# Kernel optimization log

Measured on AMD Instinct MI355X. Metric: run time of the kernel, lower is better.

The kernel has to match this reference:

```python
import jax, jax.numpy as jnp
import numpy as np

P = 2            # config['p']
BLUR = 0.05      # config['blur']
SCALING = 0.5    # config['scaling']
N_STEPS = 20     # static upper bound on the eps-annealing schedule length

N_D, N_S, D_IN, D_OUT = 2048, 1024, 768, 64


def setup_inputs() -> dict:
    key = jax.random.key(0)
    k1, k2, k3 = jax.random.split(key, 3)
    d = jax.random.normal(k1, (N_D, D_IN), dtype=jnp.float32)
    s = jax.random.normal(k2, (N_S, D_IN), dtype=jnp.float32)
    # learned projection; small init so distances (and thus the loss) stay O(1-10)
    M = 0.02 * jax.random.normal(k3, (D_IN, D_OUT), dtype=jnp.float32)
    return {"d": d, "s": s, "M": M}


def _cost(x, y):
    # geomloss p=2 cost: C(x,y) = ||x - y||^2 / 2
    x2 = jnp.sum(x * x, axis=1)[:, None]
    y2 = jnp.sum(y * y, axis=1)[None, :]
    return 0.5 * (x2 + y2 - 2.0 * (x @ y.T))


def _softmin(eps, C, h):
    # h = eps*log_weights + dual potential, shape [M]; C shape [N, M]
    return -eps * jax.nn.logsumexp((h[None, :] - C) / eps, axis=1)


def _sinkhorn_divergence(x, y):
    Na, Nb = x.shape[0], y.shape[0]
    log_a = jnp.full((Na,), -jnp.log(float(Na)), dtype=x.dtype)  # uniform weights
    log_b = jnp.full((Nb,), -jnp.log(float(Nb)), dtype=x.dtype)

    C_xy = _cost(x, y)
    C_yx = C_xy.T
    C_xx = _cost(x, x)
    C_yy = _cost(y, y)

    # geomloss max_diameter: norm of per-dim range over the union of clouds
    mins = jnp.minimum(x.min(0), y.min(0))
    maxs = jnp.maximum(x.max(0), y.max(0))
    diameter = jnp.sqrt(jnp.sum((maxs - mins) ** 2))

    # eps-scaling schedule: diameter^p -> blur^p, geometric decay by scaling^p,
    # padded to static length N_STEPS (extra steps just refine at eps=blur^p)
    t = jnp.arange(N_STEPS, dtype=x.dtype)
    eps_list = jnp.maximum((diameter ** P) * (SCALING ** P) ** t, BLUR ** P)

    eps0 = eps_list[0]
    f_ab = _softmin(eps0, C_xy, eps0 * log_b)
    g_ab = _softmin(eps0, C_yx, eps0 * log_a)
    f_aa = _softmin(eps0, C_xx, eps0 * log_a)
    g_bb = _softmin(eps0, C_yy, eps0 * log_b)

    def step(carry, eps):
        f_ab, g_ab, f_aa, g_bb = carry
        ft = _softmin(eps, C_xy, eps * log_b + g_ab)
        gt = _softmin(eps, C_yx, eps * log_a + f_ab)
        f_aa = 0.5 * (f_aa + _softmin(eps, C_xx, eps * log_a + f_aa))
        g_bb = 0.5 * (g_bb + _softmin(eps, C_yy, eps * log_b + g_bb))
        return (0.5 * (f_ab + ft), 0.5 * (g_ab + gt), f_aa, g_bb), None

    (f_ab, g_ab, f_aa, g_bb), _ = jax.lax.scan(step, (f_ab, g_ab, f_aa, g_bb), eps_list)

    # final non-averaged extrapolation step at eps = blur^p
    eps = jnp.asarray(BLUR ** P, dtype=x.dtype)
    f_ab = _softmin(eps, C_xy, eps * log_b + g_ab)
    g_ab = _softmin(eps, C_yx, eps * log_a + f_ab)
    f_aa = _softmin(eps, C_xx, eps * log_a + f_aa)
    g_bb = _softmin(eps, C_yy, eps * log_b + g_bb)

    # debiased Sinkhorn divergence: <a, f_ab - f_aa> + <b, g_ab - g_bb>
    return jnp.mean(f_ab - f_aa) + jnp.mean(g_ab - g_bb)


def reference(d, s, M):
    x = d @ M  # [N_d, D_out]
    y = s @ M  # [N_s, D_out]
    loss = _sinkhorn_divergence(x, y)
    return jnp.exp(-loss)
```

## Files before the change

### kernel.cpp

```cpp
#include <hip/hip_runtime.h>
#include <hip/hip_fp16.h>
#include <math.h>

#define ND 2048
#define NS 1024
#define DIN 768
#define DOUT 64
#define NSTEPS 20
static constexpr float BLUR2 = 0.05f * 0.05f;

#define OFF_X     0u
#define OFF_MM    199680u
#define OFF_POTS  199808u
#define POT_STRIDE 6144u
#define OFF_BARRIER 341120u
#define H_DXY 694528u
#define H_DYX 2791680u
#define H_DXX 4888832u
#define H_DYY 9083136u

#define NBLK 1152

__device__ inline unsigned fkey(float f) {
  const unsigned b = __float_as_uint(f);
  return (b & 0x80000000u) ? ~b : (b | 0x80000000u);
}
__device__ inline float funkey(unsigned k) {
  const unsigned b = (k & 0x80000000u) ? (k & 0x7FFFFFFFu) : ~k;
  return __uint_as_float(b);
}

__global__ __launch_bounds__(256) void init_mm(float* __restrict__ ws) {
  const int t = threadIdx.x;
  unsigned* mm = reinterpret_cast<unsigned*>(ws + OFF_MM);
  if (t < 64)       mm[t] = 0xFFFFFFFFu;
  else if (t < 128) mm[t] = 0u;
  unsigned* bar = reinterpret_cast<unsigned*>(ws + OFF_BARRIER);
  for (int i = t; i < 6144; i += 256) bar[i] = 0u;
}

__global__ __launch_bounds__(256) void proj_kernel(const float* __restrict__ d,
                                                   const float* __restrict__ s,
                                                   const float* __restrict__ M,
                                                   float* __restrict__ ws) {
  const int w    = threadIdx.x >> 6;
  const int lane = threadIdx.x & 63;
  const int r0   = blockIdx.x * 4;

  const float* base;
  if (r0 < ND) base = d + (size_t)r0 * DIN;
  else         base = s + (size_t)(r0 - ND) * DIN;

  const float4* s0 = reinterpret_cast<const float4*>(base + 0 * DIN + w * 192);
  const float4* s1 = reinterpret_cast<const float4*>(base + 1 * DIN + w * 192);
  const float4* s2 = reinterpret_cast<const float4*>(base + 2 * DIN + w * 192);
  const float4* s3 = reinterpret_cast<const float4*>(base + 3 * DIN + w * 192);
  const float* Mw = M + (size_t)(w * 192) * DOUT + lane;

  float a0 = 0.f, a1 = 0.f, a2 = 0.f, a3 = 0.f;
#pragma unroll 4
  for (int kk = 0; kk < 48; ++kk) {
    const float4 r0v = s0[kk];
    const float4 r1v = s1[kk];
    const float4 r2v = s2[kk];
    const float4 r3v = s3[kk];
    const float m0 = Mw[(kk * 4 + 0) * DOUT];
    const float m1 = Mw[(kk * 4 + 1) * DOUT];
    const float m2 = Mw[(kk * 4 + 2) * DOUT];
    const float m3 = Mw[(kk * 4 + 3) * DOUT];
    a0 = fmaf(r0v.x, m0, a0); a0 = fmaf(r0v.y, m1, a0);
    a0 = fmaf(r0v.z, m2, a0); a0 = fmaf(r0v.w, m3, a0);
    a1 = fmaf(r1v.x, m0, a1); a1 = fmaf(r1v.y, m1, a1);
    a1 = fmaf(r1v.z, m2, a1); a1 = fmaf(r1v.w, m3, a1);
    a2 = fmaf(r2v.x, m0, a2); a2 = fmaf(r2v.y, m1, a2);
    a2 = fmaf(r2v.z, m2, a2); a2 = fmaf(r2v.w, m3, a2);
    a3 = fmaf(r3v.x, m0, a3); a3 = fmaf(r3v.y, m1, a3);
    a3 = fmaf(r3v.z, m2, a3); a3 = fmaf(r3v.w, m3, a3);
  }

  __shared__ float part[4][4][64];
  part[w][0][lane] = a0;
  part[w][1][lane] = a1;
  part[w][2][lane] = a2;
  part[w][3][lane] = a3;
  __syncthreads();

  if (w == 0) {
    const float f0 = part[0][0][lane] + part[1][0][lane] + part[2][0][lane] + part[3][0][lane];
    const float f1 = part[0][1][lane] + part[1][1][lane] + part[2][1][lane] + part[3][1][lane];
    const float f2 = part[0][2][lane] + part[1][2][lane] + part[2][2][lane] + part[3][2][lane];
    const float f3 = part[0][3][lane] + part[1][3][lane] + part[2][3][lane] + part[3][3][lane];

    float* xy = ws + OFF_X;
    xy[(size_t)(r0 + 0) * DOUT + lane] = f0;
    xy[(size_t)(r0 + 1) * DOUT + lane] = f1;
    xy[(size_t)(r0 + 2) * DOUT + lane] = f2;
    xy[(size_t)(r0 + 3) * DOUT + lane] = f3;

    const float mn4 = fminf(fminf(f0, f1), fminf(f2, f3));
    const float mx4 = fmaxf(fmaxf(f0, f1), fmaxf(f2, f3));
    unsigned* mm = reinterpret_cast<unsigned*>(ws + OFF_MM);
    atomicMin(mm + lane, fkey(mn4));
    atomicMax(mm + 64 + lane, fkey(mx4));

    float n0 = f0 * f0, n1 = f1 * f1, n2 = f2 * f2, n3 = f3 * f3;
#pragma unroll
    for (int off = 32; off > 0; off >>= 1) {
      n0 += __shfl_xor(n0, off, 64);
      n1 += __shfl_xor(n1, off, 64);
      n2 += __shfl_xor(n2, off, 64);
      n3 += __shfl_xor(n3, off, 64);
    }
    if (lane == 0) {
      float* zp = ws + OFF_POTS;
      const float nn[4] = {0.5f * n0, 0.5f * n1, 0.5f * n2, 0.5f * n3};
#pragma unroll
      for (int k = 0; k < 4; ++k) {
        const int r = r0 + k;
        if (r < ND) { zp[r] = -nn[k];            zp[3072 + r] = -nn[k]; }
        else        { const int j = r - ND; zp[2048 + j] = -nn[k]; zp[5120 + j] = -nn[k]; }
      }
    }
  }
}

__global__ __launch_bounds__(256) void build_cost(float* __restrict__ ws) {
  const int b = blockIdx.x;
  const int tid = threadIdx.x;

  const float* A;
  const float* B;
  __half* Dout;
  __half* DoutT = nullptr;
  int ldc, ldcT = 0, ti, tj;

  const float* x = ws + OFF_X;
  const float* y = ws + OFF_X + (size_t)ND * DOUT;
  __half* hws = reinterpret_cast<__half*>(ws);

  if (b < 512) {
    ti = b >> 4; tj = b & 15;
    A = x; B = y;
    Dout = hws + H_DXY; ldc = NS;
    DoutT = hws + H_DYX; ldcT = ND;
  } else if (b < 1536) {
    const int bb = b - 512;
    ti = bb >> 5; tj = bb & 31;
    A = x; B = x;
    Dout = hws + H_DXX; ldc = ND;
  } else {
    const int bb = b - 1536;
    ti = bb >> 4; tj = bb & 15;
    A = y; B = y;
    Dout = hws + H_DYY; ldc = NS;
  }

  __shared__ float Ast[64][68];
  __shared__ float Bst[64][68];

  for (int idx = tid; idx < 64 * 16; idx += 256) {
    const int row = idx >> 4;
    const int c4 = idx & 15;
    const float4 a = reinterpret_cast<const float4*>(A + (size_t)(ti * 64 + row) * DOUT)[c4];
    Ast[c4 * 4 + 0][row] = a.x;
    Ast[c4 * 4 + 1][row] = a.y;
    Ast[c4 * 4 + 2][row] = a.z;
    Ast[c4 * 4 + 3][row] = a.w;
    const float4 bv = reinterpret_cast<const float4*>(B + (size_t)(tj * 64 + row) * DOUT)[c4];
    Bst[c4 * 4 + 0][row] = bv.x;
    Bst[c4 * 4 + 1][row] = bv.y;
    Bst[c4 * 4 + 2][row] = bv.z;
    Bst[c4 * 4 + 3][row] = bv.w;
  }
  __syncthreads();

  const int tr = tid >> 4;
  const int tc = tid & 15;
  float acc[4][4] = {};
#pragma unroll 4
  for (int k = 0; k < 64; ++k) {
    float av[4], bv[4];
#pragma unroll
    for (int i = 0; i < 4; ++i) av[i] = Ast[k][tr * 4 + i];
#pragma unroll
    for (int j = 0; j < 4; ++j) bv[j] = Bst[k][tc * 4 + j];
#pragma unroll
    for (int i = 0; i < 4; ++i)
#pragma unroll
      for (int j = 0; j < 4; ++j) acc[i][j] = fmaf(av[i], bv[j], acc[i][j]);
  }

#pragma unroll
  for (int i = 0; i < 4; ++i) {
    const int gi = ti * 64 + tr * 4 + i;
    const int col = tj * 64 + tc * 4;
    const __half h0 = __float2half_rn(acc[i][0]);
    const __half h1 = __float2half_rn(acc[i][1]);
    const __half h2 = __float2half_rn(acc[i][2]);
    const __half h3 = __float2half_rn(acc[i][3]);
    __half2* dst = reinterpret_cast<__half2*>(Dout + (size_t)gi * ldc + col);
    dst[0] = __halves2half2(h0, h1);
    dst[1] = __halves2half2(h2, h3);
    if (DoutT) {
      DoutT[(size_t)(col + 0) * ldcT + gi] = h0;
      DoutT[(size_t)(col + 1) * ldcT + gi] = h1;
      DoutT[(size_t)(col + 2) * ldcT + gi] = h2;
      DoutT[(size_t)(col + 3) * ldcT + gi] = h3;
    }
  }
}

__device__ inline void chunk_update(const float4 dv, const float4 pa, const float4 pb,
                                    float ie2, float& m, float& s) {
  const __half2* h2 = reinterpret_cast<const __half2*>(&dv);
  const float u0 = pa.x + __low2float(h2[0]), u1 = pa.y + __high2float(h2[0]);
  const float u2 = pa.z + __low2float(h2[1]), u3 = pa.w + __high2float(h2[1]);
  const float u4 = pb.x + __low2float(h2[2]), u5 = pb.y + __high2float(h2[2]);
  const float u6 = pb.z + __low2float(h2[3]), u7 = pb.w + __high2float(h2[3]);
  const float cm = fmaxf(fmaxf(fmaxf(u0, u1), fmaxf(u2, u3)),
                         fmaxf(fmaxf(u4, u5), fmaxf(u6, u7)));
  const float mn = fmaxf(m, cm);
  const float o = -mn * ie2;
  const float p0 = exp2f(fmaf(u0, ie2, o)) + exp2f(fmaf(u1, ie2, o));
  const float p1 = exp2f(fmaf(u2, ie2, o)) + exp2f(fmaf(u3, ie2, o));
  const float p2 = exp2f(fmaf(u4, ie2, o)) + exp2f(fmaf(u5, ie2, o));
  const float p3 = exp2f(fmaf(u6, ie2, o)) + exp2f(fmaf(u7, ie2, o));
  s = fmaf(s, exp2f(fmaf(m, ie2, o)), (p0 + p1) + (p2 + p3));
  m = mn;
}

__device__ inline float softmin_finish(float m, float s, float eps, float ie2,
                                       float log2N) {
  float mw = m;
#pragma unroll
  for (int off = 32; off > 0; off >>= 1) mw = fmaxf(mw, __shfl_xor(mw, off, 64));
  s *= exp2f((m - mw) * ie2);
#pragma unroll
  for (int off = 32; off > 0; off >>= 1) s += __shfl_xor(s, off, 64);
  return -mw - eps * 0.6931471806f * (log2f(s) - log2N);
}

__device__ inline float softmin_long(const __half* __restrict__ Dr,
                                     const float* __restrict__ pt,
                                     int lane, float eps, float ie2) {
  const float4* df4 = reinterpret_cast<const float4*>(Dr);
  const float4* pf4 = reinterpret_cast<const float4*>(pt);
  float mA = -3.4e38f, sA = 0.f, mB = -3.4e38f, sB = 0.f;
#pragma unroll
  for (int c = 0; c < 2; ++c) {
    const float4 dvA = df4[(2 * c + 0) * 64 + lane];
    const float4 paA = pf4[(2 * c + 0) * 128 + lane * 2];
    const float4 pbA = pf4[(2 * c + 0) * 128 + lane * 2 + 1];
    const float4 dvB = df4[(2 * c + 1) * 64 + lane];
    const float4 paB = pf4[(2 * c + 1) * 128 + lane * 2];
    const float4 pbB = pf4[(2 * c + 1) * 128 + lane * 2 + 1];
    chunk_update(dvA, paA, pbA, ie2, mA, sA);
    chunk_update(dvB, paB, pbB, ie2, mB, sB);
  }
  const float mn = fmaxf(mA, mB);
  const float s = fmaf(sA, exp2f((mA - mn) * ie2), sB * exp2f((mB - mn) * ie2));
  return softmin_finish(mn, s, eps, ie2, 11.0f);
}

__device__ inline void softmin_short2(const __half* __restrict__ Dr0,
                                      const __half* __restrict__ Dr1,
                                      const float* __restrict__ pt,
                                      int lane, float eps, float ie2,
                                      float& f0, float& f1) {
  const float4* d0 = reinterpret_cast<const float4*>(Dr0);
  const float4* d1 = reinterpret_cast<const float4*>(Dr1);
  const float4* pf4 = reinterpret_cast<const float4*>(pt);
  float m0 = -3.4e38f, s0 = 0.f, m1 = -3.4e38f, s1 = 0.f;
#pragma unroll
  for (int c = 0; c < 2; ++c) {
    const float4 pa = pf4[c * 128 + lane * 2];
    const float4 pb = pf4[c * 128 + lane * 2 + 1];
    const float4 dv0 = d0[c * 64 + lane];
    const float4 dv1 = d1[c * 64 + lane];
    chunk_update(dv0, pa, pb, ie2, m0, s0);
    chunk_update(dv1, pa, pb, ie2, m1, s1);
  }
  float mw0 = m0, mw1 = m1;
#pragma unroll
  for (int off = 32; off > 0; off >>= 1) {
    mw0 = fmaxf(mw0, __shfl_xor(mw0, off, 64));
    mw1 = fmaxf(mw1, __shfl_xor(mw1, off, 64));
  }
  s0 *= exp2f((m0 - mw0) * ie2);
  s1 *= exp2f((m1 - mw1) * ie2);
#pragma unroll
  for (int off = 32; off > 0; off >>= 1) {
    s0 += __shfl_xor(s0, off, 64);
    s1 += __shfl_xor(s1, off, 64);
  }
  f0 = -mw0 - eps * 0.6931471806f * (log2f(s0) - 10.0f);
  f1 = -mw1 - eps * 0.6931471806f * (log2f(s1) - 10.0f);
}

__device__ inline void gbarrier(unsigned* __restrict__ bar, unsigned k) {
  __syncthreads();
  if (threadIdx.x == 0) {
    unsigned* cnt = bar + (size_t)(blockIdx.x & 63) * 64;
    __hip_atomic_fetch_add(cnt, 1u, __ATOMIC_RELAXED, __HIP_MEMORY_SCOPE_SYSTEM);
  }
  if (blockIdx.x == 0) {
    if (threadIdx.x < 64) {
      const unsigned target = (unsigned)NBLK * k;
      for (;;) {
        unsigned sum = __hip_atomic_load(bar + (size_t)threadIdx.x * 64,
                                         __ATOMIC_RELAXED, __HIP_MEMORY_SCOPE_SYSTEM);
#pragma unroll
        for (int off = 32; off > 0; off >>= 1)
          sum += (unsigned)__shfl_xor((int)sum, off, 64);
        if (sum >= target) break;
        __builtin_amdgcn_s_sleep(2);
      }
      if (threadIdx.x < 32)
        __hip_atomic_store(bar + 4096 + (size_t)threadIdx.x * 64, k,
                           __ATOMIC_RELAXED, __HIP_MEMORY_SCOPE_SYSTEM);
    }
  } else {
    if (threadIdx.x == 0) {
      while (__hip_atomic_load(bar + 4096 + (size_t)(blockIdx.x & 31) * 64,
                               __ATOMIC_RELAXED, __HIP_MEMORY_SCOPE_SYSTEM) < k)
        __builtin_amdgcn_s_sleep(2);
    }
  }
  __syncthreads();
}

__global__ __launch_bounds__(256, 6) void sinkhorn_fused(float* __restrict__ ws,
                                                         float* __restrict__ out) {
  const int w    = threadIdx.x >> 6;
  const int lane = threadIdx.x & 63;
  const int W    = blockIdx.x * 4 + w;
  float* pots = ws + OFF_POTS;
  unsigned* bar = reinterpret_cast<unsigned*>(ws + OFF_BARRIER);
  const __half* hws = reinterpret_cast<const __half*>(ws);

  float diam2;
  {
    const unsigned* mm = reinterpret_cast<const unsigned*>(ws + OFF_MM);
    const float mn = funkey(mm[lane]);
    const float mx = funkey(mm[64 + lane]);
    const float rng = mx - mn;
    float p = rng * rng;
#pragma unroll
    for (int off = 32; off > 0; off >>= 1) p += __shfl_xor(p, off, 64);
    diam2 = p;
  }

  const bool isLong = (W < 3072);
  const __half* DrL = nullptr;
  int ptOffL = 0, outL = 0;
  const __half* Dr0 = nullptr;
  const __half* Dr1 = nullptr;
  int ptOffS = 0, outS0 = 0, outS1 = 0;
  if (isLong) {
    if (W < 1024) { DrL = hws + H_DYX + (size_t)W * ND;          ptOffL = 0;    }
    else          { DrL = hws + H_DXX + (size_t)(W - 1024) * ND; ptOffL = 3072; }
    outL = 2048 + W;
  } else {
    const int v = W - 3072;
    const int k0 = 2 * v;
    if (k0 < 2048) { Dr0 = hws + H_DXY + (size_t)k0 * NS; Dr1 = Dr0 + NS;
                     ptOffS = 2048; outS0 = k0; outS1 = k0 + 1; }
    else { const int r = k0 - 2048; Dr0 = hws + H_DYY + (size_t)r * NS; Dr1 = Dr0 + NS;
           ptOffS = 5120; outS0 = 5120 + r; outS1 = outS0 + 1; }
  }
  const bool isGab = isLong && (W < 1024);
  unsigned bk = 0;

  for (int t = -1; t < NSTEPS; ++t) {
    const float eps = (t < 0) ? fmaxf(diam2, BLUR2)
                              : fmaxf(ldexpf(diam2, -2 * t), BLUR2);
    const float ie2 = 1.4426950409f / eps;
    const float* pin  = pots + (size_t)(t + 1) * POT_STRIDE;
    float*       pout = pots + (size_t)(t + 2) * POT_STRIDE;
    const bool avg = (t >= 0);
    if (isLong) {
      const float prev = avg ? pin[outL] : 0.f;
      float f = softmin_long(DrL, pin + ptOffL, lane, eps, ie2);
      if (avg) f = 0.5f * (prev + f);
      if (lane == 0)
        __hip_atomic_store(&pout[outL], f, __ATOMIC_RELAXED, __HIP_MEMORY_SCOPE_AGENT);
    } else {
      const float prev0 = avg ? pin[outS0] : 0.f;
      const float prev1 = avg ? pin[outS1] : 0.f;
      float f0, f1;
      softmin_short2(Dr0, Dr1, pin + ptOffS, lane, eps, ie2, f0, f1);
      if (avg) { f0 = 0.5f * (prev0 + f0); f1 = 0.5f * (prev1 + f1); }
      if (lane == 0) {
        __hip_atomic_store(&pout[outS0], f0, __ATOMIC_RELAXED, __HIP_MEMORY_SCOPE_AGENT);
        __hip_atomic_store(&pout[outS1], f1, __ATOMIC_RELAXED, __HIP_MEMORY_SCOPE_AGENT);
      }
    }
    gbarrier(bar, ++bk);
  }

  {
    const float eps = BLUR2;
    const float ie2 = 1.4426950409f / eps;
    const float* pin  = pots + (size_t)(NSTEPS + 1) * POT_STRIDE;
    float*       pout = pots + (size_t)(NSTEPS + 2) * POT_STRIDE;
    if (isLong) {
      if (!isGab) {
        const float f = softmin_long(DrL, pin + ptOffL, lane, eps, ie2);
        if (lane == 0)
          __hip_atomic_store(&pout[outL], f, __ATOMIC_RELAXED, __HIP_MEMORY_SCOPE_AGENT);
      }
    } else {
      float f0, f1;
      softmin_short2(Dr0, Dr1, pin + ptOffS, lane, eps, ie2, f0, f1);
      if (lane == 0) {
        __hip_atomic_store(&pout[outS0], f0, __ATOMIC_RELAXED, __HIP_MEMORY_SCOPE_AGENT);
        __hip_atomic_store(&pout[outS1], f1, __ATOMIC_RELAXED, __HIP_MEMORY_SCOPE_AGENT);
      }
    }
    gbarrier(bar, ++bk);
    if (isGab) {
      const float f = softmin_long(DrL, pout + ptOffL, lane, eps, ie2);
      if (lane == 0)
        __hip_atomic_store(&pout[outL], f, __ATOMIC_RELAXED, __HIP_MEMORY_SCOPE_AGENT);
    }
    gbarrier(bar, ++bk);
  }

  if (blockIdx.x == 0) {
    const float* pot = pots + (size_t)(NSTEPS + 2) * POT_STRIDE;
    const int tid = threadIdx.x;
    float s1 = 0.f, s2 = 0.f;
    for (int i = tid; i < ND; i += 256) s1 += pot[i] - pot[3072 + i];
    for (int j = tid; j < NS; j += 256) s2 += pot[2048 + j] - pot[5120 + j];
    float part = s1 * (1.0f / (float)ND) + s2 * (1.0f / (float)NS);
#pragma unroll
    for (int off = 32; off > 0; off >>= 1) part += __shfl_xor(part, off, 64);
    __shared__ float sp[4];
    if ((tid & 63) == 0) sp[tid >> 6] = part;
    __syncthreads();
    if (tid == 0) out[0] = expf(-(sp[0] + sp[1] + sp[2] + sp[3]));
  }
}

extern "C" void kernel_launch(void* const* d_in, const int* in_sizes, int n_in,
                              void* d_out, int out_size, void* d_ws, size_t ws_size,
                              hipStream_t stream) {
  const float* d = (const float*)d_in[0];
  const float* s = (const float*)d_in[1];
  const float* M = (const float*)d_in[2];
  float* out = (float*)d_out;
  float* ws = (float*)d_ws;

  init_mm<<<1, 256, 0, stream>>>(ws);
  proj_kernel<<<768, 256, 0, stream>>>(d, s, M, ws);
  build_cost<<<1792, 256, 0, stream>>>(ws);
  sinkhorn_fused<<<NBLK, 256, 0, stream>>>(ws, out);
}
```

Measured before the change: 217.9 us.

## Split grid barrier into two independent per-wave barriers and halve block count

Replaces the block-wide grid barrier with per-wavefront arrive/poll barriers on two separate counters. One covers the cross (xy/yx) potentials and one covers the self (xx/yy) potentials. Each wave now handles one task from each group, so the grid shrinks from 1152 to 640 blocks. The A and B problems can progress with looser coupling, which removes the __syncthreads and single-detector stalls that forced every block to wait on the slowest one. The cost is more atomics per wave, more polling traffic, and more per-wave work in sequence.

```diff
diff --git a/kernel.cpp b/kernel.cpp
--- a/kernel.cpp
+++ b/kernel.cpp
@@ -13,13 +13,19 @@
 #define OFF_MM    199680u
 #define OFF_POTS  199808u
 #define POT_STRIDE 6144u
-#define OFF_BARRIER 341120u
 #define H_DXY 694528u
 #define H_DYX 2791680u
 #define H_DXX 4888832u
 #define H_DYY 9083136u
-
-#define NBLK 1152
+#define OFF_BARRIER 5066752u
+#define BAR_ARR_A 0u
+#define BAR_ARR_B 4096u
+#define BAR_GEN_A 8192u
+#define BAR_GEN_B 10240u
+
+#define NBLK 640
+#define NWA 2048u
+#define NWB 2560u
 
 __device__ inline unsigned fkey(float f) {
   const unsigned b = __float_as_uint(f);
@@ -36,7 +42,7 @@
   if (t < 64)       mm[t] = 0xFFFFFFFFu;
   else if (t < 128) mm[t] = 0u;
   unsigned* bar = reinterpret_cast<unsigned*>(ws + OFF_BARRIER);
-  for (int i = t; i < 6144; i += 256) bar[i] = 0u;
+  for (int i = t; i < 12288; i += 256) bar[i] = 0u;
 }
 
 __global__ __launch_bounds__(256) void proj_kernel(const float* __restrict__ d,
@@ -297,36 +303,33 @@
   f1 = -mw1 - eps * 0.6931471806f * (log2f(s1) - 10.0f);
 }
 
-__device__ inline void gbarrier(unsigned* __restrict__ bar, unsigned k) {
-  __syncthreads();
-  if (threadIdx.x == 0) {
-    unsigned* cnt = bar + (size_t)(blockIdx.x & 63) * 64;
-    __hip_atomic_fetch_add(cnt, 1u, __ATOMIC_RELAXED, __HIP_MEMORY_SCOPE_SYSTEM);
-  }
-  if (blockIdx.x == 0) {
-    if (threadIdx.x < 64) {
-      const unsigned target = (unsigned)NBLK * k;
-      for (;;) {
-        unsigned sum = __hip_atomic_load(bar + (size_t)threadIdx.x * 64,
-                                         __ATOMIC_RELAXED, __HIP_MEMORY_SCOPE_SYSTEM);
-#pragma unroll
-        for (int off = 32; off > 0; off >>= 1)
-          sum += (unsigned)__shfl_xor((int)sum, off, 64);
-        if (sum >= target) break;
-        __builtin_amdgcn_s_sleep(2);
-      }
-      if (threadIdx.x < 32)
-        __hip_atomic_store(bar + 4096 + (size_t)threadIdx.x * 64, k,
+__device__ inline void g_arrive(unsigned* __restrict__ bar, unsigned arrBase, int W) {
+  asm volatile("s_waitcnt vmcnt(0)" ::: "memory");
+  if ((threadIdx.x & 63) == 0)
+    __hip_atomic_fetch_add(bar + arrBase + (size_t)(W & 63) * 64, 1u,
                            __ATOMIC_RELAXED, __HIP_MEMORY_SCOPE_SYSTEM);
-    }
-  } else {
-    if (threadIdx.x == 0) {
-      while (__hip_atomic_load(bar + 4096 + (size_t)(blockIdx.x & 31) * 64,
-                               __ATOMIC_RELAXED, __HIP_MEMORY_SCOPE_SYSTEM) < k)
-        __builtin_amdgcn_s_sleep(2);
-    }
-  }
-  __syncthreads();
+}
+
+__device__ inline void g_wait_poll(const unsigned* __restrict__ genline, unsigned k) {
+  while (__hip_atomic_load(genline, __ATOMIC_RELAXED, __HIP_MEMORY_SCOPE_SYSTEM) < k)
+    __builtin_amdgcn_s_sleep(1);
+}
+
+__device__ inline void g_detect(unsigned* __restrict__ bar, unsigned arrBase,
+                                unsigned genBase, unsigned k, unsigned target) {
+  const int lane = threadIdx.x & 63;
+  for (;;) {
+    unsigned sum = __hip_atomic_load(bar + arrBase + (size_t)lane * 64,
+                                     __ATOMIC_RELAXED, __HIP_MEMORY_SCOPE_SYSTEM);
+#pragma unroll
+    for (int off = 32; off > 0; off >>= 1)
+      sum += (unsigned)__shfl_xor((int)sum, off, 64);
+    if (sum >= target) break;
+    __builtin_amdgcn_s_sleep(1);
+  }
+  if (lane < 32)
+    __hip_atomic_store(bar + genBase + (size_t)lane * 64, k,
+                       __ATOMIC_RELAXED, __HIP_MEMORY_SCOPE_SYSTEM);
 }
 
 __global__ __launch_bounds__(256, 6) void sinkhorn_fused(float* __restrict__ ws,
@@ -337,6 +340,7 @@
   float* pots = ws + OFF_POTS;
   unsigned* bar = reinterpret_cast<unsigned*>(ws + OFF_BARRIER);
   const __half* hws = reinterpret_cast<const __half*>(ws);
+  const bool detector = (W == 0);
 
   float diam2;
   {
@@ -350,52 +354,91 @@
     diam2 = p;
   }
 
-  const bool isLong = (W < 3072);
-  const __half* DrL = nullptr;
-  int ptOffL = 0, outL = 0;
-  const __half* Dr0 = nullptr;
-  const __half* Dr1 = nullptr;
-  int ptOffS = 0, outS0 = 0, outS1 = 0;
-  if (isLong) {
-    if (W < 1024) { DrL = hws + H_DYX + (size_t)W * ND;          ptOffL = 0;    }
-    else          { DrL = hws + H_DXX + (size_t)(W - 1024) * ND; ptOffL = 3072; }
-    outL = 2048 + W;
-  } else {
-    const int v = W - 3072;
-    const int k0 = 2 * v;
-    if (k0 < 2048) { Dr0 = hws + H_DXY + (size_t)k0 * NS; Dr1 = Dr0 + NS;
-                     ptOffS = 2048; outS0 = k0; outS1 = k0 + 1; }
-    else { const int r = k0 - 2048; Dr0 = hws + H_DYY + (size_t)r * NS; Dr1 = Dr0 + NS;
-           ptOffS = 5120; outS0 = 5120 + r; outS1 = outS0 + 1; }
-  }
-  const bool isGab = isLong && (W < 1024);
-  unsigned bk = 0;
-
-  for (int t = -1; t < NSTEPS; ++t) {
-    const float eps = (t < 0) ? fmaxf(diam2, BLUR2)
-                              : fmaxf(ldexpf(diam2, -2 * t), BLUR2);
+  const bool hasA  = (W < 2048);
+  const bool aLong = (W < 1024);
+  const __half* DrA0 = nullptr; const __half* DrA1 = nullptr;
+  int ptA = 0, outA0 = 0, outA1 = 0;
+  if (aLong)      { DrA0 = hws + H_DYX + (size_t)W * ND; ptA = 0; outA0 = 2048 + W; }
+  else if (hasA)  { const int u = W - 1024;
+                    DrA0 = hws + H_DXY + (size_t)(2 * u) * NS; DrA1 = DrA0 + NS;
+                    ptA = 2048; outA0 = 2 * u; outA1 = 2 * u + 1; }
+  const bool bLong = (W < 2048);
+  const __half* DrB0 = nullptr; const __half* DrB1 = nullptr;
+  int ptB = 0, outB0 = 0, outB1 = 0;
+  if (bLong) { DrB0 = hws + H_DXX + (size_t)W * ND; ptB = 3072; outB0 = 3072 + W; }
+  else       { const int v = W - 2048;
+               DrB0 = hws + H_DYY + (size_t)(2 * v) * NS; DrB1 = DrB0 + NS;
+               ptB = 5120; outB0 = 5120 + 2 * v; outB1 = outB0 + 1; }
+
+  auto computeA = [&](const float* pin, float* pout, float eps, float ie2, bool avg) {
+    if (aLong) {
+      const float prev = avg ? pin[outA0] : 0.f;
+      float f = softmin_long(DrA0, pin + ptA, lane, eps, ie2);
+      if (avg) f = 0.5f * (prev + f);
+      if (lane == 0)
+        __hip_atomic_store(&pout[outA0], f, __ATOMIC_RELAXED, __HIP_MEMORY_SCOPE_AGENT);
+    } else {
+      const float prev0 = avg ? pin[outA0] : 0.f;
+      const float prev1 = avg ? pin[outA1] : 0.f;
+      float f0, f1;
+      softmin_short2(DrA0, DrA1, pin + ptA, lane, eps, ie2, f0, f1);
+      if (avg) { f0 = 0.5f * (prev0 + f0); f1 = 0.5f * (prev1 + f1); }
+      if (lane == 0) {
+        __hip_atomic_store(&pout[outA0], f0, __ATOMIC_RELAXED, __HIP_MEMORY_SCOPE_AGENT);
+        __hip_atomic_store(&pout[outA1], f1, __ATOMIC_RELAXED, __HIP_MEMORY_SCOPE_AGENT);
+      }
+    }
+  };
+  auto computeB = [&](const float* pin, float* pout, float eps, float ie2, bool avg) {
+    if (bLong) {
+      const float prev = avg ? pin[outB0] : 0.f;
+      float f = softmin_long(DrB0, pin + ptB, lane, eps, ie2);
+      if (avg) f = 0.5f * (prev + f);
+      if (lane == 0)
+        __hip_atomic_store(&pout[outB0], f, __ATOMIC_RELAXED, __HIP_MEMORY_SCOPE_AGENT);
+    } else {
+      const float prev0 = avg ? pin[outB0] : 0.f;
+      const float prev1 = avg ? pin[outB1] : 0.f;
+      float f0, f1;
+      softmin_short2(DrB0, DrB1, pin + ptB, lane, eps, ie2, f0, f1);
+      if (avg) { f0 = 0.5f * (prev0 + f0); f1 = 0.5f * (prev1 + f1); }
+      if (lane == 0) {
+        __hip_atomic_store(&pout[outB0], f0, __ATOMIC_RELAXED, __HIP_MEMORY_SCOPE_AGENT);
+        __hip_atomic_store(&pout[outB1], f1, __ATOMIC_RELAXED, __HIP_MEMORY_SCOPE_AGENT);
+      }
+    }
+  };
+  auto waitA = [&](unsigned k) {
+    if (detector) g_detect(bar, BAR_ARR_A, BAR_GEN_A, k, NWA * k);
+    else          g_wait_poll(bar + BAR_GEN_A + (size_t)(W & 31) * 64, k);
+  };
+  auto waitB = [&](unsigned k) {
+    if (detector) g_detect(bar, BAR_ARR_B, BAR_GEN_B, k, NWB * k);
+    else          g_wait_poll(bar + BAR_GEN_B + (size_t)(W & 31) * 64, k);
+  };
+
+  {
+    const float eps = fmaxf(diam2, BLUR2);
+    const float ie2 = 1.4426950409f / eps;
+    float* pout = pots + POT_STRIDE;
+    if (hasA) { computeA(pots, pout, eps, ie2, false); g_arrive(bar, BAR_ARR_A, W); }
+    computeB(pots, pout, eps, ie2, false);
+    g_arrive(bar, BAR_ARR_B, W);
+  }
+
+  for (int t = 0; t < NSTEPS; ++t) {
+    const float eps = fmaxf(ldexpf(diam2, -2 * t), BLUR2);
     const float ie2 = 1.4426950409f / eps;
     const float* pin  = pots + (size_t)(t + 1) * POT_STRIDE;
     float*       pout = pots + (size_t)(t + 2) * POT_STRIDE;
-    const bool avg = (t >= 0);
-    if (isLong) {
-      const float prev = avg ? pin[outL] : 0.f;
-      float f = softmin_long(DrL, pin + ptOffL, lane, eps, ie2);
-      if (avg) f = 0.5f * (prev + f);
-      if (lane == 0)
-        __hip_atomic_store(&pout[outL], f, __ATOMIC_RELAXED, __HIP_MEMORY_SCOPE_AGENT);
-    } else {
-      const float prev0 = avg ? pin[outS0] : 0.f;
-      const float prev1 = avg ? pin[outS1] : 0.f;
-      float f0, f1;
-      softmin_short2(Dr0, Dr1, pin + ptOffS, lane, eps, ie2, f0, f1);
-      if (avg) { f0 = 0.5f * (prev0 + f0); f1 = 0.5f * (prev1 + f1); }
-      if (lane == 0) {
-        __hip_atomic_store(&pout[outS0], f0, __ATOMIC_RELAXED, __HIP_MEMORY_SCOPE_AGENT);
-        __hip_atomic_store(&pout[outS1], f1, __ATOMIC_RELAXED, __HIP_MEMORY_SCOPE_AGENT);
-      }
-    }
-    gbarrier(bar, ++bk);
+    if (hasA) {
+      waitA((unsigned)(t + 1));
+      computeA(pin, pout, eps, ie2, true);
+      g_arrive(bar, BAR_ARR_A, W);
+    }
+    waitB((unsigned)(t + 1));
+    computeB(pin, pout, eps, ie2, true);
+    g_arrive(bar, BAR_ARR_B, W);
   }
 
   {
@@ -403,30 +446,19 @@
     const float ie2 = 1.4426950409f / eps;
     const float* pin  = pots + (size_t)(NSTEPS + 1) * POT_STRIDE;
     float*       pout = pots + (size_t)(NSTEPS + 2) * POT_STRIDE;
-    if (isLong) {
-      if (!isGab) {
-        const float f = softmin_long(DrL, pin + ptOffL, lane, eps, ie2);
-        if (lane == 0)
-          __hip_atomic_store(&pout[outL], f, __ATOMIC_RELAXED, __HIP_MEMORY_SCOPE_AGENT);
-      }
-    } else {
-      float f0, f1;
-      softmin_short2(Dr0, Dr1, pin + ptOffS, lane, eps, ie2, f0, f1);
-      if (lane == 0) {
-        __hip_atomic_store(&pout[outS0], f0, __ATOMIC_RELAXED, __HIP_MEMORY_SCOPE_AGENT);
-        __hip_atomic_store(&pout[outS1], f1, __ATOMIC_RELAXED, __HIP_MEMORY_SCOPE_AGENT);
-      }
-    }
-    gbarrier(bar, ++bk);
-    if (isGab) {
-      const float f = softmin_long(DrL, pout + ptOffL, lane, eps, ie2);
-      if (lane == 0)
-        __hip_atomic_store(&pout[outL], f, __ATOMIC_RELAXED, __HIP_MEMORY_SCOPE_AGENT);
-    }
-    gbarrier(bar, ++bk);
+    if (hasA) waitA((unsigned)(NSTEPS + 1));
+    waitB((unsigned)(NSTEPS + 1));
+    if (hasA && !aLong) computeA(pin, pout, eps, ie2, false);
+    computeB(pin, pout, eps, ie2, false);
+    g_arrive(bar, BAR_ARR_B, W);
+    waitB((unsigned)(NSTEPS + 2));
+    if (aLong) computeA(pout, pout, eps, ie2, false);
+    g_arrive(bar, BAR_ARR_B, W);
+    waitB((unsigned)(NSTEPS + 3));
   }
 
   if (blockIdx.x == 0) {
+    __syncthreads();
     const float* pot = pots + (size_t)(NSTEPS + 2) * POT_STRIDE;
     const int tid = threadIdx.x;
     float s1 = 0.f, s2 = 0.f;
```

New measurement: 236.4 us. 1.09x slower.

## Keep cost rows in registers across steps and use decentralized grid barrier

Applied to the files above, without the earlier changes.

Each wave's fp16 cost-matrix slice is loaded once into registers before the annealing loop and reused at every Sinkhorn step, so the matrices are no longer re-read from global memory each iteration. The grid barrier changes from a master-block gather/broadcast to one where every block atomically increments one of 32 counters and then polls all of them until the total reaches the target. This drops the second broadcast hop. In exchange it adds register pressure and more polling traffic on the counters.

```diff
diff --git a/kernel.cpp b/kernel.cpp
--- a/kernel.cpp
+++ b/kernel.cpp
@@ -36,7 +36,7 @@
   if (t < 64)       mm[t] = 0xFFFFFFFFu;
   else if (t < 128) mm[t] = 0u;
   unsigned* bar = reinterpret_cast<unsigned*>(ws + OFF_BARRIER);
-  for (int i = t; i < 6144; i += 256) bar[i] = 0u;
+  for (int i = t; i < 2048; i += 256) bar[i] = 0u;
 }
 
 __global__ __launch_bounds__(256) void proj_kernel(const float* __restrict__ d,
@@ -240,45 +240,37 @@
   return -mw - eps * 0.6931471806f * (log2f(s) - log2N);
 }
 
-__device__ inline float softmin_long(const __half* __restrict__ Dr,
+__device__ inline float softmin_long(const float4 dv[4],
                                      const float* __restrict__ pt,
                                      int lane, float eps, float ie2) {
-  const float4* df4 = reinterpret_cast<const float4*>(Dr);
   const float4* pf4 = reinterpret_cast<const float4*>(pt);
   float mA = -3.4e38f, sA = 0.f, mB = -3.4e38f, sB = 0.f;
 #pragma unroll
   for (int c = 0; c < 2; ++c) {
-    const float4 dvA = df4[(2 * c + 0) * 64 + lane];
     const float4 paA = pf4[(2 * c + 0) * 128 + lane * 2];
     const float4 pbA = pf4[(2 * c + 0) * 128 + lane * 2 + 1];
-    const float4 dvB = df4[(2 * c + 1) * 64 + lane];
     const float4 paB = pf4[(2 * c + 1) * 128 + lane * 2];
     const float4 pbB = pf4[(2 * c + 1) * 128 + lane * 2 + 1];
-    chunk_update(dvA, paA, pbA, ie2, mA, sA);
-    chunk_update(dvB, paB, pbB, ie2, mB, sB);
+    chunk_update(dv[2 * c + 0], paA, pbA, ie2, mA, sA);
+    chunk_update(dv[2 * c + 1], paB, pbB, ie2, mB, sB);
   }
   const float mn = fmaxf(mA, mB);
   const float s = fmaf(sA, exp2f((mA - mn) * ie2), sB * exp2f((mB - mn) * ie2));
   return softmin_finish(mn, s, eps, ie2, 11.0f);
 }
 
-__device__ inline void softmin_short2(const __half* __restrict__ Dr0,
-                                      const __half* __restrict__ Dr1,
+__device__ inline void softmin_short2(const float4 dv[4],
                                       const float* __restrict__ pt,
                                       int lane, float eps, float ie2,
                                       float& f0, float& f1) {
-  const float4* d0 = reinterpret_cast<const float4*>(Dr0);
-  const float4* d1 = reinterpret_cast<const float4*>(Dr1);
   const float4* pf4 = reinterpret_cast<const float4*>(pt);
   float m0 = -3.4e38f, s0 = 0.f, m1 = -3.4e38f, s1 = 0.f;
 #pragma unroll
   for (int c = 0; c < 2; ++c) {
     const float4 pa = pf4[c * 128 + lane * 2];
     const float4 pb = pf4[c * 128 + lane * 2 + 1];
-    const float4 dv0 = d0[c * 64 + lane];
-    const float4 dv1 = d1[c * 64 + lane];
-    chunk_update(dv0, pa, pb, ie2, m0, s0);
-    chunk_update(dv1, pa, pb, ie2, m1, s1);
+    chunk_update(dv[c], pa, pb, ie2, m0, s0);
+    chunk_update(dv[2 + c], pa, pb, ie2, m1, s1);
   }
   float mw0 = m0, mw1 = m1;
 #pragma unroll
@@ -299,31 +291,19 @@
 
 __device__ inline void gbarrier(unsigned* __restrict__ bar, unsigned k) {
   __syncthreads();
-  if (threadIdx.x == 0) {
-    unsigned* cnt = bar + (size_t)(blockIdx.x & 63) * 64;
-    __hip_atomic_fetch_add(cnt, 1u, __ATOMIC_RELAXED, __HIP_MEMORY_SCOPE_SYSTEM);
-  }
-  if (blockIdx.x == 0) {
-    if (threadIdx.x < 64) {
-      const unsigned target = (unsigned)NBLK * k;
-      for (;;) {
-        unsigned sum = __hip_atomic_load(bar + (size_t)threadIdx.x * 64,
-                                         __ATOMIC_RELAXED, __HIP_MEMORY_SCOPE_SYSTEM);
-#pragma unroll
-        for (int off = 32; off > 0; off >>= 1)
-          sum += (unsigned)__shfl_xor((int)sum, off, 64);
-        if (sum >= target) break;
-        __builtin_amdgcn_s_sleep(2);
-      }
-      if (threadIdx.x < 32)
-        __hip_atomic_store(bar + 4096 + (size_t)threadIdx.x * 64, k,
+  if (threadIdx.x == 0)
+    __hip_atomic_fetch_add(bar + (size_t)(blockIdx.x & 31) * 64, 1u,
                            __ATOMIC_RELAXED, __HIP_MEMORY_SCOPE_SYSTEM);
-    }
-  } else {
-    if (threadIdx.x == 0) {
-      while (__hip_atomic_load(bar + 4096 + (size_t)(blockIdx.x & 31) * 64,
-                               __ATOMIC_RELAXED, __HIP_MEMORY_SCOPE_SYSTEM) < k)
-        __builtin_amdgcn_s_sleep(2);
+  if (threadIdx.x < 64) {
+    const unsigned target = 2u * (unsigned)NBLK * k;
+    for (;;) {
+      unsigned sum = __hip_atomic_load(bar + (size_t)(threadIdx.x & 31) * 64,
+                                       __ATOMIC_RELAXED, __HIP_MEMORY_SCOPE_SYSTEM);
+#pragma unroll
+      for (int off = 32; off > 0; off >>= 1)
+        sum += (unsigned)__shfl_xor((int)sum, off, 64);
+      if (sum >= target) break;
+      __builtin_amdgcn_s_sleep(1);
     }
   }
   __syncthreads();
@@ -351,25 +331,56 @@
   }
 
   const bool isLong = (W < 3072);
-  const __half* DrL = nullptr;
-  int ptOffL = 0, outL = 0;
+  const bool isGab  = (W < 1024);
+  int ptOff = 0, out0 = 0, out1 = -1;
   const __half* Dr0 = nullptr;
   const __half* Dr1 = nullptr;
-  int ptOffS = 0, outS0 = 0, outS1 = 0;
   if (isLong) {
-    if (W < 1024) { DrL = hws + H_DYX + (size_t)W * ND;          ptOffL = 0;    }
-    else          { DrL = hws + H_DXX + (size_t)(W - 1024) * ND; ptOffL = 3072; }
-    outL = 2048 + W;
+    if (isGab) { Dr0 = hws + H_DYX + (size_t)W * ND;          ptOff = 0;    }
+    else       { Dr0 = hws + H_DXX + (size_t)(W - 1024) * ND; ptOff = 3072; }
+    out0 = 2048 + W;
   } else {
     const int v = W - 3072;
     const int k0 = 2 * v;
     if (k0 < 2048) { Dr0 = hws + H_DXY + (size_t)k0 * NS; Dr1 = Dr0 + NS;
-                     ptOffS = 2048; outS0 = k0; outS1 = k0 + 1; }
+                     ptOff = 2048; out0 = k0; out1 = k0 + 1; }
     else { const int r = k0 - 2048; Dr0 = hws + H_DYY + (size_t)r * NS; Dr1 = Dr0 + NS;
-           ptOffS = 5120; outS0 = 5120 + r; outS1 = outS0 + 1; }
-  }
-  const bool isGab = isLong && (W < 1024);
+           ptOff = 5120; out0 = 5120 + r; out1 = out0 + 1; }
+  }
+
+  float4 dv[4];
+  if (isLong) {
+    const float4* df4 = reinterpret_cast<const float4*>(Dr0);
+#pragma unroll
+    for (int c = 0; c < 4; ++c) dv[c] = df4[c * 64 + lane];
+  } else {
+    const float4* d0 = reinterpret_cast<const float4*>(Dr0);
+    const float4* d1 = reinterpret_cast<const float4*>(Dr1);
+#pragma unroll
+    for (int c = 0; c < 2; ++c) { dv[c] = d0[c * 64 + lane]; dv[2 + c] = d1[c * 64 + lane]; }
+  }
+
   unsigned bk = 0;
+
+  auto doStep = [&](const float* pin, float* pout, float eps, float ie2, bool avg) {
+    if (isLong) {
+      const float prev = avg ? pin[out0] : 0.f;
+      float f = softmin_long(dv, pin + ptOff, lane, eps, ie2);
+      if (avg) f = 0.5f * (prev + f);
+      if (lane == 0)
+        __hip_atomic_store(&pout[out0], f, __ATOMIC_RELAXED, __HIP_MEMORY_SCOPE_AGENT);
+    } else {
+      const float prev0 = avg ? pin[out0] : 0.f;
+      const float prev1 = avg ? pin[out1] : 0.f;
+      float f0, f1;
+      softmin_short2(dv, pin + ptOff, lane, eps, ie2, f0, f1);
+      if (avg) { f0 = 0.5f * (prev0 + f0); f1 = 0.5f * (prev1 + f1); }
+      if (lane == 0) {
+        __hip_atomic_store(&pout[out0], f0, __ATOMIC_RELAXED, __HIP_MEMORY_SCOPE_AGENT);
+        __hip_atomic_store(&pout[out1], f1, __ATOMIC_RELAXED, __HIP_MEMORY_SCOPE_AGENT);
+      }
+    }
+  };
 
   for (int t = -1; t < NSTEPS; ++t) {
     const float eps = (t < 0) ? fmaxf(diam2, BLUR2)
@@ -377,24 +388,7 @@
     const float ie2 = 1.4426950409f / eps;
     const float* pin  = pots + (size_t)(t + 1) * POT_STRIDE;
     float*       pout = pots + (size_t)(t + 2) * POT_STRIDE;
-    const bool avg = (t >= 0);
-    if (isLong) {
-      const float prev = avg ? pin[outL] : 0.f;
-      float f = softmin_long(DrL, pin + ptOffL, lane, eps, ie2);
-      if (avg) f = 0.5f * (prev + f);
-      if (lane == 0)
-        __hip_atomic_store(&pout[outL], f, __ATOMIC_RELAXED, __HIP_MEMORY_SCOPE_AGENT);
-    } else {
-      const float prev0 = avg ? pin[outS0] : 0.f;
-      const float prev1 = avg ? pin[outS1] : 0.f;
-      float f0, f1;
-      softmin_short2(Dr0, Dr1, pin + ptOffS, lane, eps, ie2, f0, f1);
-      if (avg) { f0 = 0.5f * (prev0 + f0); f1 = 0.5f * (prev1 + f1); }
-      if (lane == 0) {
-        __hip_atomic_store(&pout[outS0], f0, __ATOMIC_RELAXED, __HIP_MEMORY_SCOPE_AGENT);
-        __hip_atomic_store(&pout[outS1], f1, __ATOMIC_RELAXED, __HIP_MEMORY_SCOPE_AGENT);
-      }
-    }
+    doStep(pin, pout, eps, ie2, t >= 0);
     gbarrier(bar, ++bk);
   }
 
@@ -403,26 +397,9 @@
     const float ie2 = 1.4426950409f / eps;
     const float* pin  = pots + (size_t)(NSTEPS + 1) * POT_STRIDE;
     float*       pout = pots + (size_t)(NSTEPS + 2) * POT_STRIDE;
-    if (isLong) {
-      if (!isGab) {
-        const float f = softmin_long(DrL, pin + ptOffL, lane, eps, ie2);
-        if (lane == 0)
-          __hip_atomic_store(&pout[outL], f, __ATOMIC_RELAXED, __HIP_MEMORY_SCOPE_AGENT);
-      }
-    } else {
-      float f0, f1;
-      softmin_short2(Dr0, Dr1, pin + ptOffS, lane, eps, ie2, f0, f1);
-      if (lane == 0) {
-        __hip_atomic_store(&pout[outS0], f0, __ATOMIC_RELAXED, __HIP_MEMORY_SCOPE_AGENT);
-        __hip_atomic_store(&pout[outS1], f1, __ATOMIC_RELAXED, __HIP_MEMORY_SCOPE_AGENT);
-      }
-    }
+    if (!isGab) doStep(pin, pout, eps, ie2, false);
     gbarrier(bar, ++bk);
-    if (isGab) {
-      const float f = softmin_long(DrL, pout + ptOffL, lane, eps, ie2);
-      if (lane == 0)
-        __hip_atomic_store(&pout[outL], f, __ATOMIC_RELAXED, __HIP_MEMORY_SCOPE_AGENT);
-    }
+    if (isGab) doStep(pout, pout, eps, ie2, false);
     gbarrier(bar, ++bk);
   }
 
```

Result: slower. 386.6 us (+77.4%).
